# Performance work log

Measured on AMD Instinct MI355X. Metric: run time of the kernel, lower is better.

Reference implementation:

```python
import jax, jax.numpy as jnp
import numpy as np

LN_EPS = 1e-5
NEG = -1e9


def _layernorm(x, g, b):
    m = jnp.mean(x, axis=-1, keepdims=True)
    v = jnp.mean(jnp.square(x - m), axis=-1, keepdims=True)
    return (x - m) * jax.lax.rsqrt(v + LN_EPS) * g + b


def setup_inputs() -> dict:
    key = jax.random.key(0)
    ks = jax.random.split(key, 16)
    B, S, E, H, D = 4, 2048, 1024, 16, 64
    s = 0.02
    return {
        "x": jax.random.normal(ks[0], (B, S, E), jnp.float32),
        "mask": jax.random.randint(ks[1], (B, S), 0, 2, jnp.int32),
        "Wq": jax.random.normal(ks[2], (H, E, D), jnp.float32) * s,
        "bq": jnp.zeros((H, D), jnp.float32),
        "Wk": jax.random.normal(ks[3], (H, E, D), jnp.float32) * s,
        "bk": jnp.zeros((H, D), jnp.float32),
        "Wv": jax.random.normal(ks[4], (H, E, D), jnp.float32) * s,
        "bv": jnp.zeros((H, D), jnp.float32),
        "Wo": jax.random.normal(ks[5], (H * D, E), jnp.float32) * s,
        "bo": jnp.zeros((E,), jnp.float32),
        "g1": jnp.ones((E,), jnp.float32),
        "b1": jnp.zeros((E,), jnp.float32),
        "W1": jax.random.normal(ks[6], (E, D), jnp.float32) * s,
        "c1": jnp.zeros((D,), jnp.float32),
        "W2": jax.random.normal(ks[7], (D, E), jnp.float32) * s,
        "c2": jnp.zeros((E,), jnp.float32),
        "g2": jnp.ones((E,), jnp.float32),
        "b2": jnp.zeros((E,), jnp.float32),
    }


def reference(x, mask, Wq, bq, Wk, bk, Wv, bv, Wo, bo, g1, b1, W1, c1, W2, c2, g2, b2):
    B, S, E = x.shape
    # per-head projections, batched over heads: [B,H,S,D]
    q = jnp.einsum('bse,hed->bhsd', x, Wq) + bq[None, :, None, :]
    k = jnp.einsum('bse,hed->bhsd', x, Wk) + bk[None, :, None, :]
    v = jnp.einsum('bse,hed->bhsd', x, Wv) + bv[None, :, None, :]
    # NOTE: original scales by sqrt(seq_len) (query.size(1)), not sqrt(head_dim)
    scale = jnp.asarray(S, x.dtype) ** 0.5
    scores = jnp.einsum('bhsd,bhtd->bhst', q, k) / scale
    scores = jnp.where(mask[:, None, None, :] == 0, NEG, scores)
    attn = jax.nn.softmax(scores, axis=-1)
    ctx = jnp.einsum('bhst,bhtd->bhsd', attn, v)
    # concat heads: [B,S,H*D]
    ctx = ctx.transpose(0, 2, 1, 3).reshape(B, S, -1)
    h = _layernorm(ctx @ Wo + bo, g1, b1)
    # bottleneck FFN (dropout = identity at eval), exact GELU
    f = jax.nn.gelu(h @ W1 + c1, approximate=False) @ W2 + c2
    # no residual connection in the original module
    return _layernorm(f, g2, b2)
```

## Files before the change

kernel.cpp:

```cpp
#include <hip/hip_runtime.h>
#include <math.h>

#define B_ 4
#define S_ 2048
#define E_ 1024
#define H_ 16
#define D_ 64
#define M_ (B_*S_)
#define QSCALE (0.022097086912079608f * 1.4426950408889634f)

typedef __bf16 bf16_t;
typedef __bf16 bf16x8 __attribute__((ext_vector_type(8)));
typedef float  f32x4  __attribute__((ext_vector_type(4)));

__device__ __forceinline__ void gload_lds16(const void* g, void* l) {
    __builtin_amdgcn_global_load_lds(
        (const __attribute__((address_space(1))) void*)g,
        (__attribute__((address_space(3))) void*)l, 16, 0, 0);
}
__device__ __forceinline__ bf16x8 ldsx8(const void* p) {
    return __builtin_bit_cast(bf16x8, *(const uint4*)p);
}
__device__ __forceinline__ unsigned short bf16bits(float x) {
    return __builtin_bit_cast(unsigned short, (bf16_t)x);
}
template<int N> __device__ __forceinline__ void waitv() {
    if constexpr (N == 8)      asm volatile("s_waitcnt vmcnt(8) lgkmcnt(0)" ::: "memory");
    else if constexpr (N == 4) asm volatile("s_waitcnt vmcnt(4) lgkmcnt(0)" ::: "memory");
    else if constexpr (N == 3) asm volatile("s_waitcnt vmcnt(3) lgkmcnt(0)" ::: "memory");
    else if constexpr (N == 2) asm volatile("s_waitcnt vmcnt(2) lgkmcnt(0)" ::: "memory");
    else                       asm volatile("s_waitcnt vmcnt(0) lgkmcnt(0)" ::: "memory");
}
__device__ __forceinline__ int fk(int row) { return ((row & 3) + 2 * ((row >> 3) & 3)) & 7; }

template<int BM, int BN, int MODE>
__global__ __launch_bounds__(256) void gemm_bf16(
    const bf16_t* __restrict__ A, const bf16_t* __restrict__ Bt,
    bf16_t* __restrict__ ob0, bf16_t* __restrict__ ob1, bf16_t* __restrict__ ob2,
    const float* __restrict__ bias0, const float* __restrict__ bias1,
    const int* __restrict__ sidx, const int* __restrict__ nkv,
    const int* __restrict__ bmap,
    int M, int N, int K)
{
    constexpr int FM = BM / 32, FN = BN / 32;
    constexpr int NL = BM / 32 + BN / 32;
    __shared__ bf16_t As[2][BM * 64];
    __shared__ bf16_t Bs[2][BN * 64];

    const int tid = threadIdx.x;
    const int w   = tid >> 6;
    const int wr  = w >> 1, wc = w & 1;
    const int lr  = tid & 15;
    const int lg  = (tid >> 4) & 3;

    int bm, bn;
    if constexpr (MODE == 2) {
        const int flat = blockIdx.y * gridDim.x + blockIdx.x;
        const int nab = nkv[4];
        if (flat >= nab * 16) return;
        const int ab  = flat % nab;
        const int col = flat / nab;
        const int ent = bmap[ab];
        bm = ((ent >> 8) << 11) + (ent & 255) * BM;
        bn = col * BN;
    } else {
        const int nwg = gridDim.x * gridDim.y;
        int bidf = blockIdx.y * gridDim.x + blockIdx.x;
        bidf = (bidf & 7) * (nwg >> 3) + (bidf >> 3);
        bm = (bidf / gridDim.x) * BM;
        bn = (bidf % gridDim.x) * BN;
    }

    int arow[FM];
    if constexpr (MODE == 2) {
        const int b2 = bm >> 11, rbase = bm & 2047;
        #pragma unroll
        for (int i = 0; i < FM; ++i) {
            const int row = (i * 256 + tid) >> 3;
            arow[i] = (b2 << 11) + sidx[(b2 << 11) + rbase + row];
        }
    } else {
        #pragma unroll
        for (int i = 0; i < FM; ++i)
            arow[i] = bm + ((i * 256 + tid) >> 3);
    }

    f32x4 acc[FM][FN] = {};

    auto STAGE = [&](int buf, int kk) {
        #pragma unroll
        for (int i = 0; i < BM / 32; ++i) {
            int idx = i * 256 + tid;
            int row = idx >> 3, slot = idx & 7;
            gload_lds16(A + (size_t)arow[i] * K + kk + (slot ^ (row & 7)) * 8,
                        (char*)As[buf] + idx * 16);
        }
        #pragma unroll
        for (int i = 0; i < BN / 32; ++i) {
            int idx = i * 256 + tid;
            int row = idx >> 3, slot = idx & 7;
            gload_lds16(Bt + (size_t)(bn + row) * K + kk + (slot ^ (row & 7)) * 8,
                        (char*)Bs[buf] + idx * 16);
        }
    };

    auto COMPUTE = [&](int buf) {
        #pragma unroll
        for (int h = 0; h < 2; ++h) {
            bf16x8 af[FM], bfr[FN];
            #pragma unroll
            for (int m = 0; m < FM; ++m) {
                int row = wr * (BM / 2) + m * 16 + lr;
                af[m] = ldsx8((char*)As[buf] + row * 128 + (((4 * h + lg) ^ (row & 7)) << 4));
            }
            #pragma unroll
            for (int n = 0; n < FN; ++n) {
                int col = wc * (BN / 2) + n * 16 + lr;
                bfr[n] = ldsx8((char*)Bs[buf] + col * 128 + (((4 * h + lg) ^ (col & 7)) << 4));
            }
            #pragma unroll
            for (int m = 0; m < FM; ++m)
                #pragma unroll
                for (int n = 0; n < FN; ++n)
                    acc[m][n] = __builtin_amdgcn_mfma_f32_16x16x32_bf16(
                        af[m], bfr[n], acc[m][n], 0, 0, 0);
        }
    };

    STAGE(0, 0);
    int cur = 0;
    for (int kk = 0; kk < K; kk += 64) {
        if (kk + 64 < K) {
            STAGE(cur ^ 1, kk + 64);
            waitv<NL>();
        } else {
            waitv<0>();
        }
        __builtin_amdgcn_s_barrier();
        COMPUTE(cur);
        __builtin_amdgcn_s_barrier();
        cur ^= 1;
    }

    #pragma unroll
    for (int n = 0; n < FN; ++n) {
        const int gcol = bn + wc * (BN / 2) + n * 16 + lr;
        if constexpr (MODE == 2) {
            const int p = gcol >> 10, nn = gcol & 1023;
            const int b2 = bm >> 11;
            const float bvl = p ? bias1[nn] : bias0[nn];
            #pragma unroll
            for (int m = 0; m < FM; ++m) {
                const int ci0 = (bm & 2047) + wr * (BM / 2) + m * 16 + lg * 4;
                if (p) {
                    ushort4 o;
                    o.x = bf16bits(acc[m][n][0] + bvl);
                    o.y = bf16bits(acc[m][n][1] + bvl);
                    o.z = bf16bits(acc[m][n][2] + bvl);
                    o.w = bf16bits(acc[m][n][3] + bvl);
                    *(ushort4*)(ob2 + ((((size_t)b2 << 10) + nn) << 11) + ci0) = o;
                } else {
                    #pragma unroll
                    for (int r = 0; r < 4; ++r)
                        ob1[((size_t)((b2 << 11) + ci0 + r) << 10) + nn] =
                            (bf16_t)(acc[m][n][r] + bvl);
                }
            }
        } else {
            const float bvl = bias0[gcol];
            #pragma unroll
            for (int m = 0; m < FM; ++m)
                #pragma unroll
                for (int r = 0; r < 4; ++r) {
                    const int grow = bm + wr * (BM / 2) + m * 16 + lg * 4 + r;
                    float v = acc[m][n][r] + bvl;
                    if constexpr (MODE == 1)
                        v = 0.5f * v * (1.0f + erff(v * 0.70710678118654752f));
                    ob0[(size_t)grow * N + gcol] = (bf16_t)v;
                }
        }
    }
}

__global__ __launch_bounds__(256) void compact_mask(
    const int* __restrict__ mask, int* __restrict__ sidx, int* __restrict__ nkv,
    int* __restrict__ bmap)
{
    __shared__ int wsum[4];
    __shared__ int nkp_s[4];
    const int tid = threadIdx.x;
    const int lane = tid & 63, wv = tid >> 6;
    const int base = tid * 8;

    for (int b = 0; b < 4; ++b) {
        int m[8], loc[8];
        int cnt = 0;
        #pragma unroll
        for (int j = 0; j < 8; ++j) {
            m[j] = mask[b * S_ + base + j];
            loc[j] = cnt;
            cnt += (m[j] != 0);
        }
        int incl = cnt;
        #pragma unroll
        for (int off = 1; off < 64; off <<= 1) {
            int t = __shfl_up(incl, off);
            if (lane >= off) incl += t;
        }
        if (lane == 63) wsum[wv] = incl;
        const int excl_lane = incl - cnt;
        __syncthreads();
        int wbase = 0;
        for (int i = 0; i < wv; ++i) wbase += wsum[i];
        const int total = wsum[0] + wsum[1] + wsum[2] + wsum[3];
        if (tid == 0) { nkv[b] = total; nkp_s[b] = (total + 127) & ~127; }
        const int tbase = wbase + excl_lane;
        #pragma unroll
        for (int j = 0; j < 8; ++j)
            if (m[j]) sidx[b * S_ + tbase + loc[j]] = base + j;
        const int nkp = (total + 127) & ~127;
        for (int c = total + tid; c < nkp; c += 256)
            sidx[b * S_ + c] = 0;
        __syncthreads();
    }

    if (tid == 0) {
        int idx = 0;
        for (int b = 0; b < 4; ++b)
            for (int rb = 0; rb < (nkp_s[b] >> 7); ++rb)
                bmap[idx++] = (b << 8) | rb;
        nkv[4] = idx;
    }
}

__global__ __launch_bounds__(512) void attn_mfma(
    const bf16_t* __restrict__ qg, const bf16_t* __restrict__ kg,
    const bf16_t* __restrict__ vg, const int* __restrict__ nkv,
    bf16_t* __restrict__ ctx)
{
    __shared__ bf16_t ks[2][64 * 64];
    __shared__ bf16_t vts[2][64 * 64];

    const int tid = threadIdx.x;
    const int w   = tid >> 6;
    const int lr  = tid & 15;
    const int lg  = (tid >> 4) & 3;

    const int bid = blockIdx.x;
    const int xcd = bid & 7, kidx = bid >> 3;
    const int bh  = xcd * 8 + (kidx >> 3);
    const int xq  = kidx & 7;
    const int b   = bh >> 4, h = bh & 15;
    const int q0w = xq * 256 + w * 32;

    const int nk = nkv[b];
    const int ntiles = (nk + 63) >> 6;
    const bool hastail = (nk & 63) != 0;

    bf16x8 aq[2][2];
    #pragma unroll
    for (int f = 0; f < 2; ++f) {
        const bf16_t* qp = qg + ((size_t)(b * S_ + q0w + f * 16 + lr) << 10) + h * 64 + lg * 8;
        aq[f][0] = ldsx8(qp);
        aq[f][1] = ldsx8(qp + 32);
    }

    bf16x8 onesf;
    {
        bf16_t o1 = (bf16_t)((lr == 0) ? 1.0f : 0.0f);
        #pragma unroll
        for (int j = 0; j < 8; ++j) onesf[j] = o1;
    }

    int koff[2][2][2], voff[2][4];
    #pragma unroll
    for (int c = 0; c < 2; ++c) {
        #pragma unroll
        for (int kf1 = 0; kf1 < 2; ++kf1) {
            const int row = c * 32 + 8 * (lr >> 2) + 4 * kf1 + (lr & 3);
            const int f = fk(row);
            koff[c][kf1][0] = row * 128 + ((lg ^ f) << 4);
            koff[c][kf1][1] = row * 128 + (((4 + lg) ^ f) << 4);
        }
        #pragma unroll
        for (int n = 0; n < 4; ++n) {
            const int rowv = n * 16 + lr;
            voff[c][n] = rowv * 128 + (((4 * c + lg) ^ (rowv & 7)) << 4);
        }
    }

    const int srow = tid >> 3, sslot = tid & 7;
    const bf16_t* kptr = kg + ((size_t)((b << 11) + srow) << 10) + h * 64
                            + (sslot ^ fk(srow)) * 8;
    const bf16_t* vptr = vg + (((size_t)bh * 64 + srow) << 11)
                            + (sslot ^ (srow & 7)) * 8;
    char* kdst = (char*)ks + tid * 16;
    char* vdst = (char*)vts + tid * 16;

    f32x4 accO[2][4] = {};
    f32x4 accL[2] = {};

    auto STAGE = [&](int buf) {
        const int nb = buf << 13;
        gload_lds16(kptr, kdst + nb);
        gload_lds16(vptr, vdst + nb);
        kptr += (size_t)64 << 10;
        vptr += 64;
    };

    auto COMPUTE = [&](int buf, int t0, bool tl) {
        const char* ksb = (const char*)ks + (buf << 13);
        const char* vsb = (const char*)vts + (buf << 13);
        #pragma unroll
        for (int c = 0; c < 2; ++c) {
            unsigned int pw0[4], pw1[4];
            #pragma unroll
            for (int kf1 = 0; kf1 < 2; ++kf1) {
                bf16x8 a0 = ldsx8(ksb + koff[c][kf1][0]);
                bf16x8 a1 = ldsx8(ksb + koff[c][kf1][1]);
                f32x4 z0 = {}, z1 = {};
                if (tl) {
                    const int keyb = t0 + c * 32 + 8 * lg + 4 * kf1;
                    f32x4 bias;
                    #pragma unroll
                    for (int r = 0; r < 4; ++r)
                        bias[r] = (keyb + r < nk) ? 0.0f : -1.0e9f;
                    z0 = bias; z1 = bias;
                }
                __builtin_amdgcn_s_setprio(1);
                z0 = __builtin_amdgcn_mfma_f32_16x16x32_bf16(a0, aq[0][0], z0, 0, 0, 0);
                z0 = __builtin_amdgcn_mfma_f32_16x16x32_bf16(a1, aq[0][1], z0, 0, 0, 0);
                z1 = __builtin_amdgcn_mfma_f32_16x16x32_bf16(a0, aq[1][0], z1, 0, 0, 0);
                z1 = __builtin_amdgcn_mfma_f32_16x16x32_bf16(a1, aq[1][1], z1, 0, 0, 0);
                __builtin_amdgcn_s_setprio(0);
                const float p00 = __builtin_amdgcn_exp2f(z0[0]);
                const float p01 = __builtin_amdgcn_exp2f(z0[1]);
                const float p02 = __builtin_amdgcn_exp2f(z0[2]);
                const float p03 = __builtin_amdgcn_exp2f(z0[3]);
                const float p10 = __builtin_amdgcn_exp2f(z1[0]);
                const float p11 = __builtin_amdgcn_exp2f(z1[1]);
                const float p12 = __builtin_amdgcn_exp2f(z1[2]);
                const float p13 = __builtin_amdgcn_exp2f(z1[3]);
                pw0[2 * kf1]     = bf16bits(p00) | ((unsigned)bf16bits(p01) << 16);
                pw0[2 * kf1 + 1] = bf16bits(p02) | ((unsigned)bf16bits(p03) << 16);
                pw1[2 * kf1]     = bf16bits(p10) | ((unsigned)bf16bits(p11) << 16);
                pw1[2 * kf1 + 1] = bf16bits(p12) | ((unsigned)bf16bits(p13) << 16);
            }
            uint4 pk0 = {pw0[0], pw0[1], pw0[2], pw0[3]};
            uint4 pk1 = {pw1[0], pw1[1], pw1[2], pw1[3]};
            const bf16x8 pa0 = __builtin_bit_cast(bf16x8, pk0);
            const bf16x8 pa1 = __builtin_bit_cast(bf16x8, pk1);

            __builtin_amdgcn_s_setprio(1);
            #pragma unroll
            for (int n = 0; n < 4; ++n) {
                bf16x8 av = ldsx8(vsb + voff[c][n]);
                accO[0][n] = __builtin_amdgcn_mfma_f32_16x16x32_bf16(av, pa0, accO[0][n], 0, 0, 0);
                accO[1][n] = __builtin_amdgcn_mfma_f32_16x16x32_bf16(av, pa1, accO[1][n], 0, 0, 0);
            }
            accL[0] = __builtin_amdgcn_mfma_f32_16x16x32_bf16(onesf, pa0, accL[0], 0, 0, 0);
            accL[1] = __builtin_amdgcn_mfma_f32_16x16x32_bf16(onesf, pa1, accL[1], 0, 0, 0);
            __builtin_amdgcn_s_setprio(0);
        }
    };

    STAGE(0);
    int cur = 0;
    for (int t = 0; t < ntiles; ++t) {
        if (t + 1 < ntiles) {
            STAGE(cur ^ 1);
            waitv<2>();
        } else {
            waitv<0>();
        }
        __builtin_amdgcn_s_barrier();
        COMPUTE(cur, t * 64, hastail && (t == ntiles - 1));
        __builtin_amdgcn_s_barrier();
        cur ^= 1;
    }

    #pragma unroll
    for (int f = 0; f < 2; ++f) {
        const float inv = 1.0f / __shfl(accL[f][0], lr);
        bf16_t* obase = ctx + ((size_t)(b * S_ + q0w + f * 16 + lr) << 10) + h * 64;
        #pragma unroll
        for (int n = 0; n < 4; ++n) {
            ushort4 o;
            o.x = bf16bits(accO[f][n][0] * inv);
            o.y = bf16bits(accO[f][n][1] * inv);
            o.z = bf16bits(accO[f][n][2] * inv);
            o.w = bf16bits(accO[f][n][3] * inv);
            *(ushort4*)(obase + n * 16 + lg * 4) = o;
        }
    }
}

__global__ __launch_bounds__(256) void prep_all(
    const float* __restrict__ x, bf16_t* __restrict__ xb,
    const float* __restrict__ Wq, const float* __restrict__ Wk,
    const float* __restrict__ Wv, bf16_t* __restrict__ WqkvT,
    const float* __restrict__ Wo, bf16_t* __restrict__ WoT,
    const float* __restrict__ W1, bf16_t* __restrict__ W1T,
    const float* __restrict__ W2, bf16_t* __restrict__ W2T,
    const float* __restrict__ bq, float* __restrict__ bqs)
{
    __shared__ float t[32][33];
    const int tid = threadIdx.x;
    int bid = blockIdx.x;

    if (bid < 4096) {
        int i = bid * 256 + tid;
        float4 a = ((const float4*)x)[i * 2];
        float4 b = ((const float4*)x)[i * 2 + 1];
        unsigned int p0 = bf16bits(a.x) | ((unsigned)bf16bits(a.y) << 16);
        unsigned int p1 = bf16bits(a.z) | ((unsigned)bf16bits(a.w) << 16);
        unsigned int p2 = bf16bits(b.x) | ((unsigned)bf16bits(b.y) << 16);
        unsigned int p3 = bf16bits(b.z) | ((unsigned)bf16bits(b.w) << 16);
        uint4 o = {p0, p1, p2, p3};
        ((uint4*)xb)[i] = o;
        return;
    }
    bid -= 4096;

    if (bid == 4224) {
        #pragma unroll
        for (int j = 0; j < 4; ++j)
            bqs[tid * 4 + j] = bq[tid * 4 + j] * QSCALE;
        return;
    }

    const float* in; bf16_t* out;
    int R, C, c0, r0;
    float scale = 1.0f;
    if (bid < 3072) {
        const int p = bid >> 10, r = bid & 1023;
        const int z = r >> 6, rem = r & 63;
        in  = (p == 0 ? Wq : p == 1 ? Wk : Wv) + z * 65536;
        out = WqkvT + p * 1048576 + z * 65536;
        R = 1024; C = 64;
        c0 = (rem & 1) * 32; r0 = (rem >> 1) * 32;
        if (p == 0) scale = QSCALE;
    } else if (bid < 4096) {
        const int r = bid - 3072;
        in = Wo; out = WoT; R = 1024; C = 1024;
        c0 = (r & 31) * 32; r0 = (r >> 5) * 32;
    } else if (bid < 4160) {
        const int r = bid - 4096;
        in = W1; out = W1T; R = 1024; C = 64;
        c0 = (r & 1) * 32; r0 = (r >> 1) * 32;
    } else {
        const int r = bid - 4160;
        in = W2; out = W2T; R = 64; C = 1024;
        c0 = (r & 31) * 32; r0 = (r >> 5) * 32;
    }

    {
        int rr = tid >> 3, c4 = (tid & 7) * 4;
        float4 v = *(const float4*)&in[(size_t)(r0 + rr) * C + c0 + c4];
        t[rr][c4 + 0] = v.x * scale;
        t[rr][c4 + 1] = v.y * scale;
        t[rr][c4 + 2] = v.z * scale;
        t[rr][c4 + 3] = v.w * scale;
    }
    __syncthreads();
    {
        int c = tid >> 3, r4 = (tid & 7) * 4;
        ushort4 o;
        o.x = bf16bits(t[r4 + 0][c]);
        o.y = bf16bits(t[r4 + 1][c]);
        o.z = bf16bits(t[r4 + 2][c]);
        o.w = bf16bits(t[r4 + 3][c]);
        *(ushort4*)(out + (size_t)(c0 + c) * R + r0 + r4) = o;
    }
}

template<typename InT, typename OutT>
__global__ __launch_bounds__(256) void ln_kernel(
    const InT* __restrict__ in, const float* __restrict__ g,
    const float* __restrict__ bta, OutT* __restrict__ out)
{
    const int row = blockIdx.x;
    const int tid = threadIdx.x;

    float x0, x1, x2, x3;
    if constexpr (sizeof(InT) == 4) {
        float4 xv = ((const float4*)(in + (size_t)row * E_))[tid];
        x0 = xv.x; x1 = xv.y; x2 = xv.z; x3 = xv.w;
    } else {
        ushort4 xv = *(const ushort4*)((const bf16_t*)in + (size_t)row * E_ + tid * 4);
        x0 = (float)__builtin_bit_cast(bf16_t, xv.x);
        x1 = (float)__builtin_bit_cast(bf16_t, xv.y);
        x2 = (float)__builtin_bit_cast(bf16_t, xv.z);
        x3 = (float)__builtin_bit_cast(bf16_t, xv.w);
    }
    float s  = x0 + x1 + x2 + x3;
    float sq = x0 * x0 + x1 * x1 + x2 * x2 + x3 * x3;
    #pragma unroll
    for (int off = 32; off > 0; off >>= 1) {
        s  += __shfl_down(s, off);
        sq += __shfl_down(sq, off);
    }
    __shared__ float ss[4], ssq[4];
    if ((tid & 63) == 0) { ss[tid >> 6] = s; ssq[tid >> 6] = sq; }
    __syncthreads();
    s  = ss[0] + ss[1] + ss[2] + ss[3];
    sq = ssq[0] + ssq[1] + ssq[2] + ssq[3];

    const float mean = s * (1.0f / E_);
    const float var  = sq * (1.0f / E_) - mean * mean;
    const float rstd = rsqrtf(var + 1e-5f);

    float4 gv = ((const float4*)g)[tid];
    float4 bv = ((const float4*)bta)[tid];
    float o0 = (x0 - mean) * rstd * gv.x + bv.x;
    float o1 = (x1 - mean) * rstd * gv.y + bv.y;
    float o2 = (x2 - mean) * rstd * gv.z + bv.z;
    float o3 = (x3 - mean) * rstd * gv.w + bv.w;
    if constexpr (sizeof(OutT) == 4) {
        float4 o = {o0, o1, o2, o3};
        ((float4*)((float*)out + (size_t)row * E_))[tid] = o;
    } else {
        ushort4 o;
        o.x = bf16bits(o0); o.y = bf16bits(o1);
        o.z = bf16bits(o2); o.w = bf16bits(o3);
        *(ushort4*)((bf16_t*)out + (size_t)row * E_ + tid * 4) = o;
    }
}

extern "C" void kernel_launch(void* const* d_in, const int* in_sizes, int n_in,
                              void* d_out, int out_size, void* d_ws, size_t ws_size,
                              hipStream_t stream)
{
    const float* x    = (const float*)d_in[0];
    const int*   mask = (const int*)d_in[1];
    const float* Wq   = (const float*)d_in[2];
    const float* bq   = (const float*)d_in[3];
    const float* Wk   = (const float*)d_in[4];
    const float* bk   = (const float*)d_in[5];
    const float* Wv   = (const float*)d_in[6];
    const float* bv   = (const float*)d_in[7];
    const float* Wo   = (const float*)d_in[8];
    const float* bo   = (const float*)d_in[9];
    const float* g1   = (const float*)d_in[10];
    const float* b1   = (const float*)d_in[11];
    const float* W1   = (const float*)d_in[12];
    const float* c1   = (const float*)d_in[13];
    const float* W2   = (const float*)d_in[14];
    const float* c2   = (const float*)d_in[15];
    const float* g2   = (const float*)d_in[16];
    const float* b2   = (const float*)d_in[17];

    char* W = (char*)d_ws;
    bf16_t* xb    = (bf16_t*)(W + 0);
    bf16_t* WqkvT = (bf16_t*)(W + 16777216);
    bf16_t* WoT   = (bf16_t*)(W + 23068672);
    bf16_t* W1T   = (bf16_t*)(W + 25165824);
    bf16_t* W2T   = (bf16_t*)(W + 25296896);
    bf16_t* qbuf  = (bf16_t*)(W + 25427968);
    bf16_t* kbuf  = (bf16_t*)(W + 42205184);
    bf16_t* vtc   = (bf16_t*)(W + 58982400);
    bf16_t* ctx   = (bf16_t*)(W + 75759616);
    bf16_t* t1b   = (bf16_t*)(W + 25427968);
    bf16_t* hb    = (bf16_t*)(W + 42205184);
    bf16_t* f1b   = (bf16_t*)(W + 0);
    bf16_t* f2b   = (bf16_t*)(W + 58982400);
    int*    sidx  = (int*)(W + 92536832);
    int*    nkv   = (int*)(W + 92569600);
    float*  bqs   = (float*)(W + 92569664);
    int*    bmap  = (int*)(W + 92573760);
    float*  out   = (float*)d_out;

    prep_all<<<8321, 256, 0, stream>>>(x, xb, Wq, Wk, Wv, WqkvT,
                                       Wo, WoT, W1, W1T, W2, W2T, bq, bqs);

    compact_mask<<<1, 256, 0, stream>>>(mask, sidx, nkv, bmap);

    gemm_bf16<128, 128, 0><<<dim3(8, 64), 256, 0, stream>>>(
        xb, WqkvT, qbuf, nullptr, nullptr, bqs, nullptr, nullptr, nullptr,
        nullptr, M_, 1024, 1024);

    gemm_bf16<128, 128, 2><<<dim3(16, 64), 256, 0, stream>>>(
        xb, WqkvT + (1 << 20), nullptr, kbuf, vtc, bk, bv, sidx, nkv,
        bmap, M_, 2048, 1024);

    attn_mfma<<<dim3(512), 512, 0, stream>>>(qbuf, kbuf, vtc, nkv, ctx);

    gemm_bf16<128, 128, 0><<<dim3(8, 64), 256, 0, stream>>>(
        ctx, WoT, t1b, nullptr, nullptr, bo, nullptr, nullptr, nullptr,
        nullptr, M_, 1024, 1024);

    ln_kernel<bf16_t, bf16_t><<<8192, 256, 0, stream>>>(t1b, g1, b1, hb);

    gemm_bf16<32, 64, 1><<<dim3(1, 256), 256, 0, stream>>>(
        hb, W1T, f1b, nullptr, nullptr, c1, nullptr, nullptr, nullptr,
        nullptr, M_, 64, 1024);

    gemm_bf16<128, 128, 0><<<dim3(8, 64), 256, 0, stream>>>(
        f1b, W2T, f2b, nullptr, nullptr, c2, nullptr, nullptr, nullptr,
        nullptr, M_, 1024, 64);

    ln_kernel<bf16_t, float><<<8192, 256, 0, stream>>>(f2b, g2, b2, out);
}
```

Baseline: 192.8 us.

## Stage MODE 2 GEMM epilogue through LDS for coalesced stores; swizzle block order

In the compacted K/V projection GEMM, the epilogue now writes bias-added bf16 results into LDS, either transposed or not depending on the output. It then copies 128x128 tiles to global memory with 16-byte vector stores, replacing scattered 2-byte and 8-byte writes. The block-to-tile mapping is also changed so that groups of 8 row blocks share a column, which should improve L2 reuse of the weight tiles. The epilogue assumes BM=BN=128 and reuses the As buffer after a barrier. It costs one extra LDS round trip and a sync.

```diff
diff --git a/kernel.cpp b/kernel.cpp
--- a/kernel.cpp
+++ b/kernel.cpp
@@ -57,9 +57,10 @@
     if constexpr (MODE == 2) {
         const int flat = blockIdx.y * gridDim.x + blockIdx.x;
         const int nab = nkv[4];
-        if (flat >= nab * 16) return;
-        const int ab  = flat % nab;
-        const int col = flat / nab;
+        const int st = flat >> 7, wfl = flat & 127;
+        const int ab = st * 8 + (wfl & 7);
+        if (ab >= nab) return;
+        const int col = wfl >> 3;
         const int ent = bmap[ab];
         bm = ((ent >> 8) << 11) + (ent & 255) * BM;
         bn = col * BN;
@@ -142,43 +143,54 @@
         cur ^= 1;
     }
 
+    if constexpr (MODE == 2) {
+        const int p = bn >> 10;
+        const int nnbase = bn & 1023;
+        const int b2 = bm >> 11;
+        const int cibase = bm & 2047;
+        bf16_t* eps = (bf16_t*)As;
+        #pragma unroll
+        for (int n = 0; n < FN; ++n) {
+            const int nn_l = wc * 64 + n * 16 + lr;
+            const float bvl = (p ? bias1 : bias0)[nnbase + nn_l];
+            #pragma unroll
+            for (int m = 0; m < FM; ++m) {
+                #pragma unroll
+                for (int r = 0; r < 4; ++r) {
+                    const int ci_l = wr * 64 + m * 16 + lg * 4 + r;
+                    const bf16_t val = (bf16_t)(acc[m][n][r] + bvl);
+                    if (p) eps[nn_l * 128 + ci_l] = val;
+                    else   eps[ci_l * 128 + nn_l] = val;
+                }
+            }
+        }
+        __syncthreads();
+        const int rowl = tid >> 1, seg = tid & 1;
+        const uint4* src = (const uint4*)(eps + rowl * 128 + seg * 64);
+        bf16_t* dst;
+        if (p)
+            dst = ob2 + (((size_t)(b2 << 10) + nnbase + rowl) << 11) + cibase + seg * 64;
+        else
+            dst = ob1 + ((size_t)((b2 << 11) + cibase + rowl) << 10) + nnbase + seg * 64;
+        #pragma unroll
+        for (int i = 0; i < 8; ++i) ((uint4*)dst)[i] = src[i];
+        return;
+    }
+
     #pragma unroll
     for (int n = 0; n < FN; ++n) {
         const int gcol = bn + wc * (BN / 2) + n * 16 + lr;
-        if constexpr (MODE == 2) {
-            const int p = gcol >> 10, nn = gcol & 1023;
-            const int b2 = bm >> 11;
-            const float bvl = p ? bias1[nn] : bias0[nn];
+        const float bvl = bias0[gcol];
+        #pragma unroll
+        for (int m = 0; m < FM; ++m)
             #pragma unroll
-            for (int m = 0; m < FM; ++m) {
-                const int ci0 = (bm & 2047) + wr * (BM / 2) + m * 16 + lg * 4;
-                if (p) {
-                    ushort4 o;
-                    o.x = bf16bits(acc[m][n][0] + bvl);
-                    o.y = bf16bits(acc[m][n][1] + bvl);
-                    o.z = bf16bits(acc[m][n][2] + bvl);
-                    o.w = bf16bits(acc[m][n][3] + bvl);
-                    *(ushort4*)(ob2 + ((((size_t)b2 << 10) + nn) << 11) + ci0) = o;
-                } else {
-                    #pragma unroll
-                    for (int r = 0; r < 4; ++r)
-                        ob1[((size_t)((b2 << 11) + ci0 + r) << 10) + nn] =
-                            (bf16_t)(acc[m][n][r] + bvl);
-                }
+            for (int r = 0; r < 4; ++r) {
+                const int grow = bm + wr * (BM / 2) + m * 16 + lg * 4 + r;
+                float v = acc[m][n][r] + bvl;
+                if constexpr (MODE == 1)
+                    v = 0.5f * v * (1.0f + erff(v * 0.70710678118654752f));
+                ob0[(size_t)grow * N + gcol] = (bf16_t)v;
             }
-        } else {
-            const float bvl = bias0[gcol];
-            #pragma unroll
-            for (int m = 0; m < FM; ++m)
-                #pragma unroll
-                for (int r = 0; r < 4; ++r) {
-                    const int grow = bm + wr * (BM / 2) + m * 16 + lg * 4 + r;
-                    float v = acc[m][n][r] + bvl;
-                    if constexpr (MODE == 1)
-                        v = 0.5f * v * (1.0f + erff(v * 0.70710678118654752f));
-                    ob0[(size_t)grow * N + gcol] = (bf16_t)v;
-                }
-        }
     }
 }
 
```

New measurement: 195.9 us. Within noise of the previous version (+1.6%).
